# Performance work log

Hardware: AMD Instinct MI355X
Metric: run time of the kernel (lower is better)

## Reference

```python
import jax, jax.numpy as jnp
import numpy as np

NEG_SLOPE = 0.2
N_NODES = 50000


def gatv2_layer(x, src, dst, Wl, Wr, att, b, concat):
    # GATv2Conv (PyG semantics): x_l = lin_l(x) feeds messages (source side),
    # x_r = lin_r(x) is the target side; attention logit per edge/head is
    # att . leaky_relu(x_l[src] + x_r[dst]); softmax over incoming edges of dst.
    H, C = att.shape
    n = x.shape[0]
    xl = (x @ Wl).reshape(n, H, C)   # [N,H,C]
    xr = (x @ Wr).reshape(n, H, C)
    h = xl[src] + xr[dst]            # [E,H,C] gather
    logits = jnp.einsum('ehc,hc->eh', jax.nn.leaky_relu(h, NEG_SLOPE), att)  # [E,H]
    # segment softmax over target nodes
    m = jax.ops.segment_max(logits, dst, num_segments=n)
    m = jnp.where(jnp.isfinite(m), m, 0.0)
    ex = jnp.exp(logits - m[dst])
    s = jax.ops.segment_sum(ex, dst, num_segments=n)
    alpha = ex / (s[dst] + 1e-16)    # [E,H]
    msg = xl[src] * alpha[:, :, None]               # [E,H,C]
    out = jax.ops.segment_sum(msg, dst, num_segments=n)  # [N,H,C] scatter-add
    out = out.reshape(n, H * C) if concat else out.mean(axis=1)
    return out + b


def setup_inputs() -> dict:
    key = jax.random.key(0)
    ks = jax.random.split(key, 10)
    in_c, out_c, heads = 128, 64, 2
    node_fts = jax.random.normal(ks[0], (N_NODES, in_c), dtype=jnp.float32)
    edge_index = jax.random.randint(ks[1], (2, 800000), 0, N_NODES, dtype=jnp.int64)
    sc = 0.1
    return {
        'node_fts': node_fts,
        'edge_index': edge_index,
        'Wl1': jax.random.normal(ks[2], (in_c, heads * out_c), dtype=jnp.float32) * sc,
        'Wr1': jax.random.normal(ks[3], (in_c, heads * out_c), dtype=jnp.float32) * sc,
        'att1': jax.random.normal(ks[4], (heads, out_c), dtype=jnp.float32) * sc,
        'b1': jnp.zeros((heads * out_c,), dtype=jnp.float32),
        'Wl2': jax.random.normal(ks[5], (heads * out_c, out_c), dtype=jnp.float32) * sc,
        'Wr2': jax.random.normal(ks[6], (heads * out_c, out_c), dtype=jnp.float32) * sc,
        'att2': jax.random.normal(ks[7], (1, out_c), dtype=jnp.float32) * sc,
        'b2': jnp.zeros((out_c,), dtype=jnp.float32),
    }


def reference(node_fts, edge_index, Wl1, Wr1, att1, b1, Wl2, Wr2, att2, b2):
    n = node_fts.shape[0]
    loop = jnp.arange(n, dtype=edge_index.dtype)  # add_self_loops=True default
    src = jnp.concatenate([edge_index[0], loop])
    dst = jnp.concatenate([edge_index[1], loop])
    x = gatv2_layer(node_fts, src, dst, Wl1, Wr1, att1, b1, concat=True)
    x = jax.nn.relu(x)
    x = gatv2_layer(x, src, dst, Wl2, Wr2, att2, b2, concat=False)
    x = jax.nn.relu(x)
    return x
```

## Files before the change

### kernel.cpp

```cpp
#include <hip/hip_runtime.h>
#include <math.h>

typedef unsigned short ush;
typedef short bf16x8 __attribute__((ext_vector_type(8)));
typedef float f32x4 __attribute__((ext_vector_type(4)));

__device__ __forceinline__ ush f2bf(float f) {
    unsigned u = __float_as_uint(f);
    u += 0x7FFFu + ((u >> 16) & 1u);
    return (ush)(u >> 16);
}
__device__ __forceinline__ float bf2f(ush u) {
    return __uint_as_float((unsigned)u << 16);
}
__device__ __forceinline__ float4 bf4_to_f4(ushort4 u) {
    float4 r;
    r.x = bf2f(u.x); r.y = bf2f(u.y); r.z = bf2f(u.z); r.w = bf2f(u.w);
    return r;
}

__global__ __launch_bounds__(256) void prep_x_k(const float* __restrict__ x,
                                                ush* __restrict__ hi,
                                                ush* __restrict__ lo, int tot4) {
    for (int i = blockIdx.x * blockDim.x + threadIdx.x; i < tot4;
         i += gridDim.x * blockDim.x) {
        const float4 v = reinterpret_cast<const float4*>(x)[i];
        ushort4 h, l4;
        h.x = f2bf(v.x); l4.x = f2bf(v.x - bf2f(h.x));
        h.y = f2bf(v.y); l4.y = f2bf(v.y - bf2f(h.y));
        h.z = f2bf(v.z); l4.z = f2bf(v.z - bf2f(h.z));
        h.w = f2bf(v.w); l4.w = f2bf(v.w - bf2f(h.w));
        reinterpret_cast<ushort4*>(hi)[i] = h;
        reinterpret_cast<ushort4*>(lo)[i] = l4;
    }
}

__global__ __launch_bounds__(64) void prep_w_k(
    const float* __restrict__ Wl1, const float* __restrict__ Wr1,
    const float* __restrict__ Wl2, const float* __restrict__ Wr2,
    ush* __restrict__ wph, ush* __restrict__ wpl) {
    const int bid = blockIdx.x, l = threadIdx.x;
    const float* W;
    int C, fid;
    if (bid < 32)      { W = Wl1; C = 128; fid = bid; }
    else if (bid < 64) { W = Wr1; C = 128; fid = bid - 32; }
    else if (bid < 80) { W = Wl2; C = 64;  fid = bid - 64; }
    else               { W = Wr2; C = 64;  fid = bid - 80; }
    const int nc16 = C / 16;
    const int ks = fid / nc16, c16 = fid % nc16;
#pragma unroll
    for (int j = 0; j < 8; ++j) {
        const int k = ks * 32 + (l >> 4) * 8 + j;
        const int c = c16 * 16 + (l & 15);
        const float v = W[(size_t)k * C + c];
        const ush h = f2bf(v);
        wph[(size_t)(bid * 64 + l) * 8 + j] = h;
        wpl[(size_t)(bid * 64 + l) * 8 + j] = f2bf(v - bf2f(h));
    }
}

template <int CW>
__global__ __launch_bounds__(256) void gemm_mfma_k(
    const ush* __restrict__ xhi, const ush* __restrict__ xlo,
    const ush* __restrict__ wh1, const ush* __restrict__ wl1,
    const ush* __restrict__ wh2, const ush* __restrict__ wl2,
    ush* __restrict__ ybf, float* __restrict__ yf, int n) {
    constexpr int NC16 = CW / 16;
    constexpr int SPW = CW / 64;
    const int l = threadIdx.x & 63;
    const int w = threadIdx.x >> 6;
    const int r0 = blockIdx.x * 64 + w * 16;
    const int slab = blockIdx.y;
    const bool isW1 = slab < SPW;
    const int slab_local = isW1 ? slab : slab - SPW;
    const ush* __restrict__ wh = isW1 ? wh1 : wh2;
    const ush* __restrict__ wl = isW1 ? wl1 : wl2;

    const int arow = min(r0 + (l & 15), n - 1);
    const int kb = (l >> 4) * 8;
    bf16x8 ah[4], al[4];
#pragma unroll
    for (int ks = 0; ks < 4; ++ks) {
        ah[ks] = *reinterpret_cast<const bf16x8*>(xhi + (size_t)arow * 128 + ks * 32 + kb);
        al[ks] = *reinterpret_cast<const bf16x8*>(xlo + (size_t)arow * 128 + ks * 32 + kb);
    }
    const int drow = (l >> 4) * 4;
    const int dcol = l & 15;
#pragma unroll
    for (int c16 = 0; c16 < 4; ++c16) {
        f32x4 acc = {0.f, 0.f, 0.f, 0.f};
#pragma unroll
        for (int ks = 0; ks < 4; ++ks) {
            const int fid = ks * NC16 + slab_local * 4 + c16;
            const bf16x8 bh = *reinterpret_cast<const bf16x8*>(wh + (size_t)(fid * 64 + l) * 8);
            const bf16x8 bl = *reinterpret_cast<const bf16x8*>(wl + (size_t)(fid * 64 + l) * 8);
            acc = __builtin_amdgcn_mfma_f32_16x16x32_bf16(ah[ks], bh, acc, 0, 0, 0);
            acc = __builtin_amdgcn_mfma_f32_16x16x32_bf16(al[ks], bh, acc, 0, 0, 0);
            acc = __builtin_amdgcn_mfma_f32_16x16x32_bf16(ah[ks], bl, acc, 0, 0, 0);
        }
        const int cg = slab_local * 64 + c16 * 16 + dcol;
#pragma unroll
        for (int q = 0; q < 4; ++q) {
            const int gr = r0 + drow + q;
            if (gr < n) {
                if (isW1) ybf[(size_t)gr * CW + cg] = f2bf(acc[q]);
                else      yf[(size_t)gr * CW + cg] = acc[q];
            }
        }
    }
}


__global__ __launch_bounds__(256) void hist_k(const int* __restrict__ dsts,
                                              int* __restrict__ ghist,
                                              int e0, int etot) {
    __shared__ int h[512];
    const int t = threadIdx.x;
    for (int i = t; i < 512; i += 256) h[i] = 0;
    __syncthreads();
    for (int i = blockIdx.x * blockDim.x + t; i < etot; i += gridDim.x * blockDim.x) {
        const int d = (i < e0) ? dsts[i] : (i - e0);
        atomicAdd(&h[d >> 7], 1);
    }
    __syncthreads();
    for (int i = t; i < 512; i += 256)
        if (h[i]) atomicAdd(&ghist[i], h[i]);
}

__global__ __launch_bounds__(512) void scanb_k(const int* __restrict__ ghist,
                                               int* __restrict__ boff,
                                               int* __restrict__ cur) {
    __shared__ int red[512];
    const int t = threadIdx.x;
    const int x = ghist[t];
    red[t] = x;
    __syncthreads();
#pragma unroll
    for (int s = 1; s < 512; s <<= 1) {
        const int add = (t >= s) ? red[t - s] : 0;
        __syncthreads();
        red[t] += add;
        __syncthreads();
    }
    const int excl = red[t] - x;
    boff[t] = excl;
    cur[t] = excl;
}

__global__ __launch_bounds__(256) void semisort_k(
    const int* __restrict__ srcs, const int* __restrict__ dsts,
    int* __restrict__ cur, int2* __restrict__ pairs, int e0, int etot) {
    __shared__ int hist[512], gbase[512], lcur[512];
    const int t = threadIdx.x;
    const int start = blockIdx.x * 2048;
    const int end = min(start + 2048, etot);
    for (int i = t; i < 512; i += 256) { hist[i] = 0; lcur[i] = 0; }
    __syncthreads();
    for (int i = start + t; i < end; i += 256) {
        const int d = (i < e0) ? dsts[i] : (i - e0);
        atomicAdd(&hist[d >> 7], 1);
    }
    __syncthreads();
    for (int i = t; i < 512; i += 256) {
        const int c = hist[i];
        gbase[i] = c ? atomicAdd(&cur[i], c) : 0;
    }
    __syncthreads();
    for (int i = start + t; i < end; i += 256) {
        int s, d;
        if (i < e0) { s = srcs[i]; d = dsts[i]; } else { s = d = i - e0; }
        const int b = d >> 7;
        const int p = atomicAdd(&lcur[b], 1);
        int2 pr; pr.x = s; pr.y = d;
        pairs[gbase[b] + p] = pr;
    }
}

__global__ __launch_bounds__(256) void bucket_fill_k(
    const int2* __restrict__ pairs, const int* __restrict__ boff,
    int* __restrict__ row_ptr, int* __restrict__ csr_src, int n, int etot) {
    __shared__ int cnt[128], cur[128];
    const int b = blockIdx.x, t = threadIdx.x;
    const int lo = boff[b], hi = boff[b + 1];
    if (t < 128) cnt[t] = 0;
    __syncthreads();
    for (int e = lo + t; e < hi; e += 256)
        atomicAdd(&cnt[pairs[e].y & 127], 1);
    __syncthreads();
    const int x = (t < 128) ? cnt[t] : 0;
#pragma unroll
    for (int s = 1; s < 128; s <<= 1) {
        const int add = (t < 128 && t >= s) ? cnt[t - s] : 0;
        __syncthreads();
        if (t < 128) cnt[t] += add;
        __syncthreads();
    }
    if (t < 128) {
        const int excl = cnt[t] - x;
        cur[t] = excl;
        const int d = b * 128 + t;
        if (d < n) row_ptr[d] = lo + excl;
    }
    if (b == 0 && t == 0) row_ptr[n] = etot;
    __syncthreads();
    for (int e = lo + t; e < hi; e += 256) {
        const int2 p = pairs[e];
        const int pos = atomicAdd(&cur[p.y & 127], 1);
        csr_src[lo + pos] = p.x;
    }
}

__global__ __launch_bounds__(256) void gat_dst2_k(
    const ush* __restrict__ xl, const float* __restrict__ xr,
    const int* __restrict__ row_ptr, const int* __restrict__ csr_src,
    const float* __restrict__ att, const float* __restrict__ bias,
    ush* __restrict__ h1hi, ush* __restrict__ h1lo, int n) {
    const int lane = threadIdx.x & 63;
    const int g = lane >> 5, l32 = lane & 31;
    const int d = (blockIdx.x * blockDim.x + threadIdx.x) >> 6;
    if (d >= n) return;

    const float4 xrv = reinterpret_cast<const float4*>(xr + (size_t)d * 128)[l32];
    const float4 atv = reinterpret_cast<const float4*>(att)[l32];
    const int rp0 = row_ptr[d], rp1 = row_ptr[d + 1];

    float s = 0.f;
    float4 acc = {0.f, 0.f, 0.f, 0.f};
    int i = rp0 + g;
    for (; i + 2 < rp1; i += 4) {
        const int s0 = csr_src[i];
        const int s1 = csr_src[i + 2];
        const float4 a0 = bf4_to_f4(reinterpret_cast<const ushort4*>(xl + (size_t)s0 * 128)[l32]);
        const float4 a1 = bf4_to_f4(reinterpret_cast<const ushort4*>(xl + (size_t)s1 * 128)[l32]);
        float v, p0 = 0.f, p1 = 0.f;
        v = a0.x + xrv.x; p0 = fmaf(atv.x, (v > 0.f ? v : 0.2f * v), p0);
        v = a0.y + xrv.y; p0 = fmaf(atv.y, (v > 0.f ? v : 0.2f * v), p0);
        v = a0.z + xrv.z; p0 = fmaf(atv.z, (v > 0.f ? v : 0.2f * v), p0);
        v = a0.w + xrv.w; p0 = fmaf(atv.w, (v > 0.f ? v : 0.2f * v), p0);
        v = a1.x + xrv.x; p1 = fmaf(atv.x, (v > 0.f ? v : 0.2f * v), p1);
        v = a1.y + xrv.y; p1 = fmaf(atv.y, (v > 0.f ? v : 0.2f * v), p1);
        v = a1.z + xrv.z; p1 = fmaf(atv.z, (v > 0.f ? v : 0.2f * v), p1);
        v = a1.w + xrv.w; p1 = fmaf(atv.w, (v > 0.f ? v : 0.2f * v), p1);
#pragma unroll
        for (int msk = 8; msk >= 1; msk >>= 1) {
            p0 += __shfl_xor(p0, msk, 64);
            p1 += __shfl_xor(p1, msk, 64);
        }
        const float w0 = __expf(p0), w1 = __expf(p1);
        s += w0 + w1;
        acc.x = fmaf(w0, a0.x, fmaf(w1, a1.x, acc.x));
        acc.y = fmaf(w0, a0.y, fmaf(w1, a1.y, acc.y));
        acc.z = fmaf(w0, a0.z, fmaf(w1, a1.z, acc.z));
        acc.w = fmaf(w0, a0.w, fmaf(w1, a1.w, acc.w));
    }
    if (i < rp1) {
        const int s0 = csr_src[i];
        const float4 a0 = bf4_to_f4(reinterpret_cast<const ushort4*>(xl + (size_t)s0 * 128)[l32]);
        float v, p0 = 0.f;
        v = a0.x + xrv.x; p0 = fmaf(atv.x, (v > 0.f ? v : 0.2f * v), p0);
        v = a0.y + xrv.y; p0 = fmaf(atv.y, (v > 0.f ? v : 0.2f * v), p0);
        v = a0.z + xrv.z; p0 = fmaf(atv.z, (v > 0.f ? v : 0.2f * v), p0);
        v = a0.w + xrv.w; p0 = fmaf(atv.w, (v > 0.f ? v : 0.2f * v), p0);
#pragma unroll
        for (int msk = 8; msk >= 1; msk >>= 1) p0 += __shfl_xor(p0, msk, 64);
        const float w0 = __expf(p0);
        s += w0;
        acc.x = fmaf(w0, a0.x, acc.x);
        acc.y = fmaf(w0, a0.y, acc.y);
        acc.z = fmaf(w0, a0.z, acc.z);
        acc.w = fmaf(w0, a0.w, acc.w);
    }
    s += __shfl_xor(s, 32, 64);
    acc.x += __shfl_xor(acc.x, 32, 64);
    acc.y += __shfl_xor(acc.y, 32, 64);
    acc.z += __shfl_xor(acc.z, 32, 64);
    acc.w += __shfl_xor(acc.w, 32, 64);
    if (g == 0) {
        const float inv = 1.f / (s + 1e-16f);
        const float4 bv = reinterpret_cast<const float4*>(bias)[l32];
        float4 o;
        o.x = fmaxf(fmaf(acc.x, inv, bv.x), 0.f);
        o.y = fmaxf(fmaf(acc.y, inv, bv.y), 0.f);
        o.z = fmaxf(fmaf(acc.z, inv, bv.z), 0.f);
        o.w = fmaxf(fmaf(acc.w, inv, bv.w), 0.f);
        ushort4 hh, ll;
        hh.x = f2bf(o.x); ll.x = f2bf(o.x - bf2f(hh.x));
        hh.y = f2bf(o.y); ll.y = f2bf(o.y - bf2f(hh.y));
        hh.z = f2bf(o.z); ll.z = f2bf(o.z - bf2f(hh.z));
        hh.w = f2bf(o.w); ll.w = f2bf(o.w - bf2f(hh.w));
        reinterpret_cast<ushort4*>(h1hi + (size_t)d * 128)[l32] = hh;
        reinterpret_cast<ushort4*>(h1lo + (size_t)d * 128)[l32] = ll;
    }
}

__global__ __launch_bounds__(256) void gat_dst1_k(
    const ush* __restrict__ xl, const float* __restrict__ xr,
    const int* __restrict__ row_ptr, const int* __restrict__ csr_src,
    const float* __restrict__ att, const float* __restrict__ bias,
    float* __restrict__ out, int n) {
    const int lane = threadIdx.x & 63;
    const int g = lane >> 4, l16 = lane & 15;
    const int d = (blockIdx.x * blockDim.x + threadIdx.x) >> 6;
    if (d >= n) return;

    const float4 xrv = reinterpret_cast<const float4*>(xr + (size_t)d * 64)[l16];
    const float4 atv = reinterpret_cast<const float4*>(att)[l16];
    const int rp0 = row_ptr[d], rp1 = row_ptr[d + 1];

    float s = 0.f;
    float4 acc = {0.f, 0.f, 0.f, 0.f};
    int i = rp0 + g;
    for (; i + 4 < rp1; i += 8) {
        const int s0 = csr_src[i];
        const int s1 = csr_src[i + 4];
        const float4 a0 = bf4_to_f4(reinterpret_cast<const ushort4*>(xl + (size_t)s0 * 64)[l16]);
        const float4 a1 = bf4_to_f4(reinterpret_cast<const ushort4*>(xl + (size_t)s1 * 64)[l16]);
        float v, p0 = 0.f, p1 = 0.f;
        v = a0.x + xrv.x; p0 = fmaf(atv.x, (v > 0.f ? v : 0.2f * v), p0);
        v = a0.y + xrv.y; p0 = fmaf(atv.y, (v > 0.f ? v : 0.2f * v), p0);
        v = a0.z + xrv.z; p0 = fmaf(atv.z, (v > 0.f ? v : 0.2f * v), p0);
        v = a0.w + xrv.w; p0 = fmaf(atv.w, (v > 0.f ? v : 0.2f * v), p0);
        v = a1.x + xrv.x; p1 = fmaf(atv.x, (v > 0.f ? v : 0.2f * v), p1);
        v = a1.y + xrv.y; p1 = fmaf(atv.y, (v > 0.f ? v : 0.2f * v), p1);
        v = a1.z + xrv.z; p1 = fmaf(atv.z, (v > 0.f ? v : 0.2f * v), p1);
        v = a1.w + xrv.w; p1 = fmaf(atv.w, (v > 0.f ? v : 0.2f * v), p1);
#pragma unroll
        for (int msk = 8; msk >= 1; msk >>= 1) {
            p0 += __shfl_xor(p0, msk, 64);
            p1 += __shfl_xor(p1, msk, 64);
        }
        const float w0 = __expf(p0), w1 = __expf(p1);
        s += w0 + w1;
        acc.x = fmaf(w0, a0.x, fmaf(w1, a1.x, acc.x));
        acc.y = fmaf(w0, a0.y, fmaf(w1, a1.y, acc.y));
        acc.z = fmaf(w0, a0.z, fmaf(w1, a1.z, acc.z));
        acc.w = fmaf(w0, a0.w, fmaf(w1, a1.w, acc.w));
    }
    if (i < rp1) {
        const int s0 = csr_src[i];
        const float4 a0 = bf4_to_f4(reinterpret_cast<const ushort4*>(xl + (size_t)s0 * 64)[l16]);
        float v, p0 = 0.f;
        v = a0.x + xrv.x; p0 = fmaf(atv.x, (v > 0.f ? v : 0.2f * v), p0);
        v = a0.y + xrv.y; p0 = fmaf(atv.y, (v > 0.f ? v : 0.2f * v), p0);
        v = a0.z + xrv.z; p0 = fmaf(atv.z, (v > 0.f ? v : 0.2f * v), p0);
        v = a0.w + xrv.w; p0 = fmaf(atv.w, (v > 0.f ? v : 0.2f * v), p0);
#pragma unroll
        for (int msk = 8; msk >= 1; msk >>= 1) p0 += __shfl_xor(p0, msk, 64);
        const float w0 = __expf(p0);
        s += w0;
        acc.x = fmaf(w0, a0.x, acc.x);
        acc.y = fmaf(w0, a0.y, acc.y);
        acc.z = fmaf(w0, a0.z, acc.z);
        acc.w = fmaf(w0, a0.w, acc.w);
    }
#pragma unroll
    for (int off = 16; off <= 32; off <<= 1) {
        s += __shfl_xor(s, off, 64);
        acc.x += __shfl_xor(acc.x, off, 64);
        acc.y += __shfl_xor(acc.y, off, 64);
        acc.z += __shfl_xor(acc.z, off, 64);
        acc.w += __shfl_xor(acc.w, off, 64);
    }
    if (g == 0) {
        const float inv = 1.f / (s + 1e-16f);
        const float4 bv = reinterpret_cast<const float4*>(bias)[l16];
        float4 o;
        o.x = fmaxf(fmaf(acc.x, inv, bv.x), 0.f);
        o.y = fmaxf(fmaf(acc.y, inv, bv.y), 0.f);
        o.z = fmaxf(fmaf(acc.z, inv, bv.z), 0.f);
        o.w = fmaxf(fmaf(acc.w, inv, bv.w), 0.f);
        reinterpret_cast<float4*>(out + (size_t)d * 64)[l16] = o;
    }
}

extern "C" void kernel_launch(void* const* d_in, const int* in_sizes, int n_in,
                              void* d_out, int out_size, void* d_ws, size_t ws_size,
                              hipStream_t stream) {
    const float* x    = (const float*)d_in[0];
    const int*   ei   = (const int*)d_in[1];
    const float* Wl1  = (const float*)d_in[2];
    const float* Wr1  = (const float*)d_in[3];
    const float* att1 = (const float*)d_in[4];
    const float* b1   = (const float*)d_in[5];
    const float* Wl2  = (const float*)d_in[6];
    const float* Wr2  = (const float*)d_in[7];
    const float* att2 = (const float*)d_in[8];
    const float* b2   = (const float*)d_in[9];

    const int n    = in_sizes[0] / 128;
    const int e0   = in_sizes[1] / 2;
    const int etot = e0 + n;
    const int* srcs = ei;
    const int* dsts = ei + e0;

    float* ws = (float*)d_ws;
    ush*   xhi  = (ush*)ws;
    ush*   xlo  = (ush*)(ws + (size_t)n * 64);
    ush*   xlbf = (ush*)(ws + (size_t)n * 128);
    float* xr   = ws + (size_t)n * 192;
    int* row_ptr = (int*)(ws + (size_t)n * 320);
    int* ghist   = row_ptr + (n + 2);
    int* boff    = ghist + 512;
    int* cur     = boff + 512;
    int* csr_src = cur + 512;
    int2* pairs  = (int2*)(csr_src + etot);
    ush* wph     = (ush*)(pairs + etot);
    ush* wpl     = wph + 96 * 512;

    const int NB = (n + 127) / 128;
    const int nblka = (etot + 2047) / 2048;

    hipMemsetAsync(ghist, 0, 512 * sizeof(int), stream);
    hist_k<<<256, 256, 0, stream>>>(dsts, ghist, e0, etot);
    scanb_k<<<1, 512, 0, stream>>>(ghist, boff, cur);
    semisort_k<<<nblka, 256, 0, stream>>>(srcs, dsts, cur, pairs, e0, etot);
    bucket_fill_k<<<NB, 256, 0, stream>>>(pairs, boff, row_ptr, csr_src, n, etot);

    prep_w_k<<<96, 64, 0, stream>>>(Wl1, Wr1, Wl2, Wr2, wph, wpl);
    prep_x_k<<<2048, 256, 0, stream>>>(x, xhi, xlo, n * 32);

    const int gx = (n + 63) / 64;

    gemm_mfma_k<128><<<dim3(gx, 4), 256, 0, stream>>>(
        xhi, xlo, wph, wpl, wph + 32 * 512, wpl + 32 * 512, xlbf, xr, n);
    gat_dst2_k<<<(n + 3) / 4, 256, 0, stream>>>(xlbf, xr, row_ptr, csr_src,
                                                att1, b1, xhi, xlo, n);

    gemm_mfma_k<64><<<dim3(gx, 2), 256, 0, stream>>>(
        xhi, xlo, wph + 64 * 512, wpl + 64 * 512, wph + 80 * 512, wpl + 80 * 512,
        xlbf, xr, n);
    gat_dst1_k<<<(n + 3) / 4, 256, 0, stream>>>(xlbf, xr, row_ptr, csr_src,
                                                att2, b2, (float*)d_out, n);
}
```

Baseline: 198.2 us.

## Sort destination nodes by degree and widen per-lane gather to 8 bf16

Adds a degree histogram, scan and ordering pass so that the two GAT aggregation kernels process destinations in descending-degree order, grouping similar-length rows into the same wavefront and block. The aggregation kernels also switch to 16-byte per-lane loads of 8 bf16 values with more edges processed in parallel per wave (4 groups for layer 1, 8 for layer 2) and shorter shuffle reductions. This targets load imbalance and the number of memory transactions per gathered row. In exchange it adds two small kernels and an atomic scatter, and it loses destination locality for the xr reads and output writes.

```diff
diff --git a/kernel.cpp b/kernel.cpp
--- a/kernel.cpp
+++ b/kernel.cpp
@@ -4,6 +4,7 @@
 typedef unsigned short ush;
 typedef short bf16x8 __attribute__((ext_vector_type(8)));
 typedef float f32x4 __attribute__((ext_vector_type(4)));
+typedef ush ushx8 __attribute__((ext_vector_type(8)));
 
 __device__ __forceinline__ ush f2bf(float f) {
     unsigned u = __float_as_uint(f);
@@ -12,11 +13,6 @@
 }
 __device__ __forceinline__ float bf2f(ush u) {
     return __uint_as_float((unsigned)u << 16);
-}
-__device__ __forceinline__ float4 bf4_to_f4(ushort4 u) {
-    float4 r;
-    r.x = bf2f(u.x); r.y = bf2f(u.y); r.z = bf2f(u.z); r.w = bf2f(u.w);
-    return r;
 }
 
 __global__ __launch_bounds__(256) void prep_x_k(const float* __restrict__ x,
@@ -110,7 +106,6 @@
     }
 }
 
-
 __global__ __launch_bounds__(256) void hist_k(const int* __restrict__ dsts,
                                               int* __restrict__ ghist,
                                               int e0, int etot) {
@@ -178,7 +173,8 @@
 
 __global__ __launch_bounds__(256) void bucket_fill_k(
     const int2* __restrict__ pairs, const int* __restrict__ boff,
-    int* __restrict__ row_ptr, int* __restrict__ csr_src, int n, int etot) {
+    int* __restrict__ row_ptr, int* __restrict__ csr_src,
+    int* __restrict__ dbin, int n, int etot) {
     __shared__ int cnt[128], cur[128];
     const int b = blockIdx.x, t = threadIdx.x;
     const int lo = boff[b], hi = boff[b + 1];
@@ -199,7 +195,10 @@
         const int excl = cnt[t] - x;
         cur[t] = excl;
         const int d = b * 128 + t;
-        if (d < n) row_ptr[d] = lo + excl;
+        if (d < n) {
+            row_ptr[d] = lo + excl;
+            atomicAdd(&dbin[127 - min(x, 127)], 1);
+        }
     }
     if (b == 0 && t == 0) row_ptr[n] = etot;
     __syncthreads();
@@ -210,166 +209,224 @@
     }
 }
 
+__global__ __launch_bounds__(128) void deg_scan_k(const int* __restrict__ dbin,
+                                                  int* __restrict__ dcur) {
+    __shared__ int red[128];
+    const int t = threadIdx.x;
+    const int x = dbin[t];
+    red[t] = x;
+    __syncthreads();
+#pragma unroll
+    for (int s = 1; s < 128; s <<= 1) {
+        const int add = (t >= s) ? red[t - s] : 0;
+        __syncthreads();
+        red[t] += add;
+        __syncthreads();
+    }
+    dcur[t] = red[t] - x;
+}
+
+__global__ __launch_bounds__(256) void deg_order_k(const int* __restrict__ row_ptr,
+                                                   int* __restrict__ dcur,
+                                                   int* __restrict__ order, int n) {
+    for (int d = blockIdx.x * blockDim.x + threadIdx.x; d < n;
+         d += gridDim.x * blockDim.x) {
+        const int deg = row_ptr[d + 1] - row_ptr[d];
+        const int pos = atomicAdd(&dcur[127 - min(deg, 127)], 1);
+        order[pos] = d;
+    }
+}
+
 __global__ __launch_bounds__(256) void gat_dst2_k(
     const ush* __restrict__ xl, const float* __restrict__ xr,
     const int* __restrict__ row_ptr, const int* __restrict__ csr_src,
-    const float* __restrict__ att, const float* __restrict__ bias,
-    ush* __restrict__ h1hi, ush* __restrict__ h1lo, int n) {
+    const int* __restrict__ order, const float* __restrict__ att,
+    const float* __restrict__ bias, ush* __restrict__ h1hi,
+    ush* __restrict__ h1lo, int n) {
     const int lane = threadIdx.x & 63;
-    const int g = lane >> 5, l32 = lane & 31;
-    const int d = (blockIdx.x * blockDim.x + threadIdx.x) >> 6;
-    if (d >= n) return;
-
-    const float4 xrv = reinterpret_cast<const float4*>(xr + (size_t)d * 128)[l32];
-    const float4 atv = reinterpret_cast<const float4*>(att)[l32];
+    const int g = lane >> 4, il = lane & 15;
+    const int w = (blockIdx.x * blockDim.x + threadIdx.x) >> 6;
+    if (w >= n) return;
+    const int d = order[w];
+
+    float xv[8], av[8];
+    {
+        const float4* xp = reinterpret_cast<const float4*>(xr + (size_t)d * 128 + il * 8);
+        const float4* ap = reinterpret_cast<const float4*>(att + il * 8);
+        const float4 x0 = xp[0], x1 = xp[1], a0 = ap[0], a1 = ap[1];
+        xv[0]=x0.x; xv[1]=x0.y; xv[2]=x0.z; xv[3]=x0.w;
+        xv[4]=x1.x; xv[5]=x1.y; xv[6]=x1.z; xv[7]=x1.w;
+        av[0]=a0.x; av[1]=a0.y; av[2]=a0.z; av[3]=a0.w;
+        av[4]=a1.x; av[5]=a1.y; av[6]=a1.z; av[7]=a1.w;
+    }
     const int rp0 = row_ptr[d], rp1 = row_ptr[d + 1];
 
     float s = 0.f;
-    float4 acc = {0.f, 0.f, 0.f, 0.f};
-    int i = rp0 + g;
-    for (; i + 2 < rp1; i += 4) {
-        const int s0 = csr_src[i];
-        const int s1 = csr_src[i + 2];
-        const float4 a0 = bf4_to_f4(reinterpret_cast<const ushort4*>(xl + (size_t)s0 * 128)[l32]);
-        const float4 a1 = bf4_to_f4(reinterpret_cast<const ushort4*>(xl + (size_t)s1 * 128)[l32]);
-        float v, p0 = 0.f, p1 = 0.f;
-        v = a0.x + xrv.x; p0 = fmaf(atv.x, (v > 0.f ? v : 0.2f * v), p0);
-        v = a0.y + xrv.y; p0 = fmaf(atv.y, (v > 0.f ? v : 0.2f * v), p0);
-        v = a0.z + xrv.z; p0 = fmaf(atv.z, (v > 0.f ? v : 0.2f * v), p0);
-        v = a0.w + xrv.w; p0 = fmaf(atv.w, (v > 0.f ? v : 0.2f * v), p0);
-        v = a1.x + xrv.x; p1 = fmaf(atv.x, (v > 0.f ? v : 0.2f * v), p1);
-        v = a1.y + xrv.y; p1 = fmaf(atv.y, (v > 0.f ? v : 0.2f * v), p1);
-        v = a1.z + xrv.z; p1 = fmaf(atv.z, (v > 0.f ? v : 0.2f * v), p1);
-        v = a1.w + xrv.w; p1 = fmaf(atv.w, (v > 0.f ? v : 0.2f * v), p1);
-#pragma unroll
-        for (int msk = 8; msk >= 1; msk >>= 1) {
-            p0 += __shfl_xor(p0, msk, 64);
-            p1 += __shfl_xor(p1, msk, 64);
-        }
-        const float w0 = __expf(p0), w1 = __expf(p1);
-        s += w0 + w1;
-        acc.x = fmaf(w0, a0.x, fmaf(w1, a1.x, acc.x));
-        acc.y = fmaf(w0, a0.y, fmaf(w1, a1.y, acc.y));
-        acc.z = fmaf(w0, a0.z, fmaf(w1, a1.z, acc.z));
-        acc.w = fmaf(w0, a0.w, fmaf(w1, a1.w, acc.w));
-    }
-    if (i < rp1) {
-        const int s0 = csr_src[i];
-        const float4 a0 = bf4_to_f4(reinterpret_cast<const ushort4*>(xl + (size_t)s0 * 128)[l32]);
-        float v, p0 = 0.f;
-        v = a0.x + xrv.x; p0 = fmaf(atv.x, (v > 0.f ? v : 0.2f * v), p0);
-        v = a0.y + xrv.y; p0 = fmaf(atv.y, (v > 0.f ? v : 0.2f * v), p0);
-        v = a0.z + xrv.z; p0 = fmaf(atv.z, (v > 0.f ? v : 0.2f * v), p0);
-        v = a0.w + xrv.w; p0 = fmaf(atv.w, (v > 0.f ? v : 0.2f * v), p0);
-#pragma unroll
-        for (int msk = 8; msk >= 1; msk >>= 1) p0 += __shfl_xor(p0, msk, 64);
-        const float w0 = __expf(p0);
-        s += w0;
-        acc.x = fmaf(w0, a0.x, acc.x);
-        acc.y = fmaf(w0, a0.y, acc.y);
-        acc.z = fmaf(w0, a0.z, acc.z);
-        acc.w = fmaf(w0, a0.w, acc.w);
-    }
-    s += __shfl_xor(s, 32, 64);
-    acc.x += __shfl_xor(acc.x, 32, 64);
-    acc.y += __shfl_xor(acc.y, 32, 64);
-    acc.z += __shfl_xor(acc.z, 32, 64);
-    acc.w += __shfl_xor(acc.w, 32, 64);
-    if (g == 0) {
-        const float inv = 1.f / (s + 1e-16f);
-        const float4 bv = reinterpret_cast<const float4*>(bias)[l32];
-        float4 o;
-        o.x = fmaxf(fmaf(acc.x, inv, bv.x), 0.f);
-        o.y = fmaxf(fmaf(acc.y, inv, bv.y), 0.f);
-        o.z = fmaxf(fmaf(acc.z, inv, bv.z), 0.f);
-        o.w = fmaxf(fmaf(acc.w, inv, bv.w), 0.f);
-        ushort4 hh, ll;
-        hh.x = f2bf(o.x); ll.x = f2bf(o.x - bf2f(hh.x));
-        hh.y = f2bf(o.y); ll.y = f2bf(o.y - bf2f(hh.y));
-        hh.z = f2bf(o.z); ll.z = f2bf(o.z - bf2f(hh.z));
-        hh.w = f2bf(o.w); ll.w = f2bf(o.w - bf2f(hh.w));
-        reinterpret_cast<ushort4*>(h1hi + (size_t)d * 128)[l32] = hh;
-        reinterpret_cast<ushort4*>(h1lo + (size_t)d * 128)[l32] = ll;
-    }
-}
-
-__global__ __launch_bounds__(256) void gat_dst1_k(
-    const ush* __restrict__ xl, const float* __restrict__ xr,
-    const int* __restrict__ row_ptr, const int* __restrict__ csr_src,
-    const float* __restrict__ att, const float* __restrict__ bias,
-    float* __restrict__ out, int n) {
-    const int lane = threadIdx.x & 63;
-    const int g = lane >> 4, l16 = lane & 15;
-    const int d = (blockIdx.x * blockDim.x + threadIdx.x) >> 6;
-    if (d >= n) return;
-
-    const float4 xrv = reinterpret_cast<const float4*>(xr + (size_t)d * 64)[l16];
-    const float4 atv = reinterpret_cast<const float4*>(att)[l16];
-    const int rp0 = row_ptr[d], rp1 = row_ptr[d + 1];
-
-    float s = 0.f;
-    float4 acc = {0.f, 0.f, 0.f, 0.f};
+    float acc[8] = {0.f, 0.f, 0.f, 0.f, 0.f, 0.f, 0.f, 0.f};
     int i = rp0 + g;
     for (; i + 4 < rp1; i += 8) {
         const int s0 = csr_src[i];
         const int s1 = csr_src[i + 4];
-        const float4 a0 = bf4_to_f4(reinterpret_cast<const ushort4*>(xl + (size_t)s0 * 64)[l16]);
-        const float4 a1 = bf4_to_f4(reinterpret_cast<const ushort4*>(xl + (size_t)s1 * 64)[l16]);
-        float v, p0 = 0.f, p1 = 0.f;
-        v = a0.x + xrv.x; p0 = fmaf(atv.x, (v > 0.f ? v : 0.2f * v), p0);
-        v = a0.y + xrv.y; p0 = fmaf(atv.y, (v > 0.f ? v : 0.2f * v), p0);
-        v = a0.z + xrv.z; p0 = fmaf(atv.z, (v > 0.f ? v : 0.2f * v), p0);
-        v = a0.w + xrv.w; p0 = fmaf(atv.w, (v > 0.f ? v : 0.2f * v), p0);
-        v = a1.x + xrv.x; p1 = fmaf(atv.x, (v > 0.f ? v : 0.2f * v), p1);
-        v = a1.y + xrv.y; p1 = fmaf(atv.y, (v > 0.f ? v : 0.2f * v), p1);
-        v = a1.z + xrv.z; p1 = fmaf(atv.z, (v > 0.f ? v : 0.2f * v), p1);
-        v = a1.w + xrv.w; p1 = fmaf(atv.w, (v > 0.f ? v : 0.2f * v), p1);
-#pragma unroll
-        for (int msk = 8; msk >= 1; msk >>= 1) {
-            p0 += __shfl_xor(p0, msk, 64);
-            p1 += __shfl_xor(p1, msk, 64);
-        }
+        const ushx8 u0 = *reinterpret_cast<const ushx8*>(xl + (((size_t)(unsigned)s0) << 7) + il * 8);
+        const ushx8 u1 = *reinterpret_cast<const ushx8*>(xl + (((size_t)(unsigned)s1) << 7) + il * 8);
+        float f0[8], f1[8], p0 = 0.f, p1 = 0.f;
+#pragma unroll
+        for (int j = 0; j < 8; ++j) {
+            f0[j] = bf2f((ush)u0[j]);
+            const float v = f0[j] + xv[j];
+            p0 = fmaf(av[j], fmaxf(v, 0.2f * v), p0);
+        }
+#pragma unroll
+        for (int j = 0; j < 8; ++j) {
+            f1[j] = bf2f((ush)u1[j]);
+            const float v = f1[j] + xv[j];
+            p1 = fmaf(av[j], fmaxf(v, 0.2f * v), p1);
+        }
+        p0 += __shfl_xor(p0, 4, 64); p0 += __shfl_xor(p0, 2, 64); p0 += __shfl_xor(p0, 1, 64);
+        p1 += __shfl_xor(p1, 4, 64); p1 += __shfl_xor(p1, 2, 64); p1 += __shfl_xor(p1, 1, 64);
         const float w0 = __expf(p0), w1 = __expf(p1);
         s += w0 + w1;
-        acc.x = fmaf(w0, a0.x, fmaf(w1, a1.x, acc.x));
-        acc.y = fmaf(w0, a0.y, fmaf(w1, a1.y, acc.y));
-        acc.z = fmaf(w0, a0.z, fmaf(w1, a1.z, acc.z));
-        acc.w = fmaf(w0, a0.w, fmaf(w1, a1.w, acc.w));
+#pragma unroll
+        for (int j = 0; j < 8; ++j) acc[j] = fmaf(w0, f0[j], fmaf(w1, f1[j], acc[j]));
     }
     if (i < rp1) {
         const int s0 = csr_src[i];
-        const float4 a0 = bf4_to_f4(reinterpret_cast<const ushort4*>(xl + (size_t)s0 * 64)[l16]);
-        float v, p0 = 0.f;
-        v = a0.x + xrv.x; p0 = fmaf(atv.x, (v > 0.f ? v : 0.2f * v), p0);
-        v = a0.y + xrv.y; p0 = fmaf(atv.y, (v > 0.f ? v : 0.2f * v), p0);
-        v = a0.z + xrv.z; p0 = fmaf(atv.z, (v > 0.f ? v : 0.2f * v), p0);
-        v = a0.w + xrv.w; p0 = fmaf(atv.w, (v > 0.f ? v : 0.2f * v), p0);
-#pragma unroll
-        for (int msk = 8; msk >= 1; msk >>= 1) p0 += __shfl_xor(p0, msk, 64);
+        const ushx8 u0 = *reinterpret_cast<const ushx8*>(xl + (((size_t)(unsigned)s0) << 7) + il * 8);
+        float f0[8], p0 = 0.f;
+#pragma unroll
+        for (int j = 0; j < 8; ++j) {
+            f0[j] = bf2f((ush)u0[j]);
+            const float v = f0[j] + xv[j];
+            p0 = fmaf(av[j], fmaxf(v, 0.2f * v), p0);
+        }
+        p0 += __shfl_xor(p0, 4, 64); p0 += __shfl_xor(p0, 2, 64); p0 += __shfl_xor(p0, 1, 64);
         const float w0 = __expf(p0);
         s += w0;
-        acc.x = fmaf(w0, a0.x, acc.x);
-        acc.y = fmaf(w0, a0.y, acc.y);
-        acc.z = fmaf(w0, a0.z, acc.z);
-        acc.w = fmaf(w0, a0.w, acc.w);
+#pragma unroll
+        for (int j = 0; j < 8; ++j) acc[j] = fmaf(w0, f0[j], acc[j]);
     }
 #pragma unroll
     for (int off = 16; off <= 32; off <<= 1) {
         s += __shfl_xor(s, off, 64);
-        acc.x += __shfl_xor(acc.x, off, 64);
-        acc.y += __shfl_xor(acc.y, off, 64);
-        acc.z += __shfl_xor(acc.z, off, 64);
-        acc.w += __shfl_xor(acc.w, off, 64);
+#pragma unroll
+        for (int j = 0; j < 8; ++j) acc[j] += __shfl_xor(acc[j], off, 64);
     }
     if (g == 0) {
         const float inv = 1.f / (s + 1e-16f);
-        const float4 bv = reinterpret_cast<const float4*>(bias)[l16];
-        float4 o;
-        o.x = fmaxf(fmaf(acc.x, inv, bv.x), 0.f);
-        o.y = fmaxf(fmaf(acc.y, inv, bv.y), 0.f);
-        o.z = fmaxf(fmaf(acc.z, inv, bv.z), 0.f);
-        o.w = fmaxf(fmaf(acc.w, inv, bv.w), 0.f);
-        reinterpret_cast<float4*>(out + (size_t)d * 64)[l16] = o;
+        float bv[8];
+        {
+            const float4* bp = reinterpret_cast<const float4*>(bias + il * 8);
+            const float4 b0 = bp[0], b1 = bp[1];
+            bv[0]=b0.x; bv[1]=b0.y; bv[2]=b0.z; bv[3]=b0.w;
+            bv[4]=b1.x; bv[5]=b1.y; bv[6]=b1.z; bv[7]=b1.w;
+        }
+        ushx8 hh, ll;
+#pragma unroll
+        for (int j = 0; j < 8; ++j) {
+            const float o = fmaxf(fmaf(acc[j], inv, bv[j]), 0.f);
+            const ush h = f2bf(o);
+            hh[j] = h;
+            ll[j] = f2bf(o - bf2f(h));
+        }
+        *reinterpret_cast<ushx8*>(h1hi + (size_t)d * 128 + il * 8) = hh;
+        *reinterpret_cast<ushx8*>(h1lo + (size_t)d * 128 + il * 8) = ll;
+    }
+}
+
+__global__ __launch_bounds__(256) void gat_dst1_k(
+    const ush* __restrict__ xl, const float* __restrict__ xr,
+    const int* __restrict__ row_ptr, const int* __restrict__ csr_src,
+    const int* __restrict__ order, const float* __restrict__ att,
+    const float* __restrict__ bias, float* __restrict__ out, int n) {
+    const int lane = threadIdx.x & 63;
+    const int g = lane >> 3, il = lane & 7;
+    const int w = (blockIdx.x * blockDim.x + threadIdx.x) >> 6;
+    if (w >= n) return;
+    const int d = order[w];
+
+    float xv[8], av[8];
+    {
+        const float4* xp = reinterpret_cast<const float4*>(xr + (size_t)d * 64 + il * 8);
+        const float4* ap = reinterpret_cast<const float4*>(att + il * 8);
+        const float4 x0 = xp[0], x1 = xp[1], a0 = ap[0], a1 = ap[1];
+        xv[0]=x0.x; xv[1]=x0.y; xv[2]=x0.z; xv[3]=x0.w;
+        xv[4]=x1.x; xv[5]=x1.y; xv[6]=x1.z; xv[7]=x1.w;
+        av[0]=a0.x; av[1]=a0.y; av[2]=a0.z; av[3]=a0.w;
+        av[4]=a1.x; av[5]=a1.y; av[6]=a1.z; av[7]=a1.w;
+    }
+    const int rp0 = row_ptr[d], rp1 = row_ptr[d + 1];
+
+    float s = 0.f;
+    float acc[8] = {0.f, 0.f, 0.f, 0.f, 0.f, 0.f, 0.f, 0.f};
+    int i = rp0 + g;
+    for (; i + 8 < rp1; i += 16) {
+        const int s0 = csr_src[i];
+        const int s1 = csr_src[i + 8];
+        const ushx8 u0 = *reinterpret_cast<const ushx8*>(xl + (((size_t)(unsigned)s0) << 6) + il * 8);
+        const ushx8 u1 = *reinterpret_cast<const ushx8*>(xl + (((size_t)(unsigned)s1) << 6) + il * 8);
+        float f0[8], f1[8], p0 = 0.f, p1 = 0.f;
+#pragma unroll
+        for (int j = 0; j < 8; ++j) {
+            f0[j] = bf2f((ush)u0[j]);
+            const float v = f0[j] + xv[j];
+            p0 = fmaf(av[j], fmaxf(v, 0.2f * v), p0);
+        }
+#pragma unroll
+        for (int j = 0; j < 8; ++j) {
+            f1[j] = bf2f((ush)u1[j]);
+            const float v = f1[j] + xv[j];
+            p1 = fmaf(av[j], fmaxf(v, 0.2f * v), p1);
+        }
+        p0 += __shfl_xor(p0, 4, 64); p0 += __shfl_xor(p0, 2, 64); p0 += __shfl_xor(p0, 1, 64);
+        p1 += __shfl_xor(p1, 4, 64); p1 += __shfl_xor(p1, 2, 64); p1 += __shfl_xor(p1, 1, 64);
+        const float w0 = __expf(p0), w1 = __expf(p1);
+        s += w0 + w1;
+#pragma unroll
+        for (int j = 0; j < 8; ++j) acc[j] = fmaf(w0, f0[j], fmaf(w1, f1[j], acc[j]));
+    }
+    if (i < rp1) {
+        const int s0 = csr_src[i];
+        const ushx8 u0 = *reinterpret_cast<const ushx8*>(xl + (((size_t)(unsigned)s0) << 6) + il * 8);
+        float f0[8], p0 = 0.f;
+#pragma unroll
+        for (int j = 0; j < 8; ++j) {
+            f0[j] = bf2f((ush)u0[j]);
+            const float v = f0[j] + xv[j];
+            p0 = fmaf(av[j], fmaxf(v, 0.2f * v), p0);
+        }
+        p0 += __shfl_xor(p0, 4, 64); p0 += __shfl_xor(p0, 2, 64); p0 += __shfl_xor(p0, 1, 64);
+        const float w0 = __expf(p0);
+        s += w0;
+#pragma unroll
+        for (int j = 0; j < 8; ++j) acc[j] = fmaf(w0, f0[j], acc[j]);
+    }
+#pragma unroll
+    for (int off = 8; off <= 32; off <<= 1) {
+        s += __shfl_xor(s, off, 64);
+#pragma unroll
+        for (int j = 0; j < 8; ++j) acc[j] += __shfl_xor(acc[j], off, 64);
+    }
+    if (g == 0) {
+        const float inv = 1.f / (s + 1e-16f);
+        float bv[8];
+        {
+            const float4* bp = reinterpret_cast<const float4*>(bias + il * 8);
+            const float4 b0 = bp[0], b1 = bp[1];
+            bv[0]=b0.x; bv[1]=b0.y; bv[2]=b0.z; bv[3]=b0.w;
+            bv[4]=b1.x; bv[5]=b1.y; bv[6]=b1.z; bv[7]=b1.w;
+        }
+        float4 o0, o1;
+        o0.x = fmaxf(fmaf(acc[0], inv, bv[0]), 0.f);
+        o0.y = fmaxf(fmaf(acc[1], inv, bv[1]), 0.f);
+        o0.z = fmaxf(fmaf(acc[2], inv, bv[2]), 0.f);
+        o0.w = fmaxf(fmaf(acc[3], inv, bv[3]), 0.f);
+        o1.x = fmaxf(fmaf(acc[4], inv, bv[4]), 0.f);
+        o1.y = fmaxf(fmaf(acc[5], inv, bv[5]), 0.f);
+        o1.z = fmaxf(fmaf(acc[6], inv, bv[6]), 0.f);
+        o1.w = fmaxf(fmaf(acc[7], inv, bv[7]), 0.f);
+        float4* op = reinterpret_cast<float4*>(out + (size_t)d * 64 + il * 8);
+        op[0] = o0;
+        op[1] = o1;
     }
 }
 
@@ -400,9 +457,12 @@
     float* xr   = ws + (size_t)n * 192;
     int* row_ptr = (int*)(ws + (size_t)n * 320);
     int* ghist   = row_ptr + (n + 2);
-    int* boff    = ghist + 512;
+    int* dbin    = ghist + 512;
+    int* dcur    = dbin + 128;
+    int* boff    = dcur + 128;
     int* cur     = boff + 512;
-    int* csr_src = cur + 512;
+    int* order   = cur + 512;
+    int* csr_src = order + n;
     int2* pairs  = (int2*)(csr_src + etot);
     ush* wph     = (ush*)(pairs + etot);
     ush* wpl     = wph + 96 * 512;
@@ -410,11 +470,13 @@
     const int NB = (n + 127) / 128;
     const int nblka = (etot + 2047) / 2048;
 
-    hipMemsetAsync(ghist, 0, 512 * sizeof(int), stream);
+    hipMemsetAsync(ghist, 0, 640 * sizeof(int), stream);
     hist_k<<<256, 256, 0, stream>>>(dsts, ghist, e0, etot);
     scanb_k<<<1, 512, 0, stream>>>(ghist, boff, cur);
     semisort_k<<<nblka, 256, 0, stream>>>(srcs, dsts, cur, pairs, e0, etot);
-    bucket_fill_k<<<NB, 256, 0, stream>>>(pairs, boff, row_ptr, csr_src, n, etot);
+    bucket_fill_k<<<NB, 256, 0, stream>>>(pairs, boff, row_ptr, csr_src, dbin, n, etot);
+    deg_scan_k<<<1, 128, 0, stream>>>(dbin, dcur);
+    deg_order_k<<<196, 256, 0, stream>>>(row_ptr, dcur, order, n);
 
     prep_w_k<<<96, 64, 0, stream>>>(Wl1, Wr1, Wl2, Wr2, wph, wpl);
     prep_x_k<<<2048, 256, 0, stream>>>(x, xhi, xlo, n * 32);
@@ -423,12 +485,12 @@
 
     gemm_mfma_k<128><<<dim3(gx, 4), 256, 0, stream>>>(
         xhi, xlo, wph, wpl, wph + 32 * 512, wpl + 32 * 512, xlbf, xr, n);
-    gat_dst2_k<<<(n + 3) / 4, 256, 0, stream>>>(xlbf, xr, row_ptr, csr_src,
+    gat_dst2_k<<<(n + 3) / 4, 256, 0, stream>>>(xlbf, xr, row_ptr, csr_src, order,
                                                 att1, b1, xhi, xlo, n);
 
     gemm_mfma_k<64><<<dim3(gx, 2), 256, 0, stream>>>(
         xhi, xlo, wph + 64 * 512, wpl + 64 * 512, wph + 80 * 512, wpl + 80 * 512,
         xlbf, xr, n);
-    gat_dst1_k<<<(n + 3) / 4, 256, 0, stream>>>(xlbf, xr, row_ptr, csr_src,
+    gat_dst1_k<<<(n + 3) / 4, 256, 0, stream>>>(xlbf, xr, row_ptr, csr_src, order,
                                                 att2, b2, (float*)d_out, n);
 }
```

After: 424.9 us. 114% more time.
